# Optimization experiments

Hardware: AMD Instinct MI355X
Metric: run time of the kernel (lower is better)

## Reference

```python
import jax, jax.numpy as jnp
import numpy as np

NUM_HEADS = 8
MASK_RATE = 0.5


def setup_inputs() -> dict:
    key = jax.random.key(0)
    ks = jax.random.split(key, 6)
    B, N, C = 8, 1024, 256
    TABLE = 10
    att_embedding = jax.random.normal(ks[0], (B, N, C), dtype=jnp.float32)
    relation_position = jax.random.randint(ks[1], (B, N, N), 0, TABLE, dtype=jnp.int32)
    rel_len = jax.random.randint(ks[2], (B,), 0, 20, dtype=jnp.int32)
    W_qkv = jax.random.normal(ks[3], (C, 3 * C), dtype=jnp.float32) * (1.0 / np.sqrt(C))
    W_proj = jax.random.normal(ks[4], (C, C), dtype=jnp.float32) * (1.0 / np.sqrt(C))
    b_proj = jnp.zeros((C,), dtype=jnp.float32)
    bias_table = jax.random.normal(ks[5], (TABLE, NUM_HEADS), dtype=jnp.float32) * 0.02
    return {
        "att_embedding": att_embedding,
        "relation_position": relation_position,
        "rel_len": rel_len,
        "W_qkv": W_qkv,
        "W_proj": W_proj,
        "b_proj": b_proj,
        "bias_table": bias_table,
    }


def reference(att_embedding, relation_position, rel_len, W_qkv, W_proj, b_proj, bias_table):
    B, N, C = att_embedding.shape
    H = NUM_HEADS
    hd = C // H
    scale = hd ** -0.5

    # QKV projection (no bias): [B,N,3C] -> q,k,v each [B,H,N,hd]
    qkv = (att_embedding @ W_qkv).reshape(B, N, 3, H, hd)
    qkv = jnp.transpose(qkv, (2, 0, 3, 1, 4))
    q, k, v = qkv[0], qkv[1], qkv[2]

    # Attention scores [B,H,N,N]
    attn = jnp.einsum("bhnd,bhmd->bhnm", q, k) * scale

    # Relative position bias: gather [B,N,N,H] -> [B,H,N,N]
    pos_bias = jnp.transpose(bias_table[relation_position], (0, 3, 1, 2))

    # Mask bias: table row t gets -100 iff t > mask_len (mask_len+1 .. TABLE-1);
    # identical across heads -> compute as [B,1,N,N] instead of materializing [B,H,N,N].
    mask_len = (rel_len.astype(jnp.float32) * MASK_RATE).astype(jnp.int32)
    mask_bias = jnp.where(relation_position > mask_len[:, None, None], -100.0, 0.0)[:, None]

    attn = jax.nn.softmax(attn + pos_bias + mask_bias, axis=-1)

    # Weighted values -> [B,N,C] -> output projection
    x = jnp.einsum("bhnm,bhmd->bnhd", attn, v).reshape(B, N, C)
    x = x @ W_proj + b_proj
    return x
```

## Files before the change

kernel.cpp:

```cpp
#include <hip/hip_runtime.h>
#include <hip/hip_bf16.h>

typedef __bf16 bf16;
typedef __bf16 bf16x2 __attribute__((ext_vector_type(2)));
typedef __bf16 bf16x8 __attribute__((ext_vector_type(8)));
typedef float f32x4 __attribute__((ext_vector_type(4)));
typedef int i32x4 __attribute__((ext_vector_type(4)));

#define B_ 8
#define N_ 1024
#define C_ 256
#define H_ 8
#define C3_ 768
#define SCALE 0.17677669529663689f
#define FMAX 16.0f


__global__ __launch_bounds__(256) void prep(
    const float* __restrict__ Wqkv, const float* __restrict__ Wproj,
    bf16* __restrict__ Wq_tiled, bf16* __restrict__ Wp_tiled)
{
  int bb = blockIdx.x;
  int o = bb * 256 + threadIdx.x;
  if (bb < 768) {
    int kk = o & 31;
    int idx = o >> 5;
    int nr = idx & 63;
    int qq = idx >> 6;
    int nt = qq % 12, kt = qq / 12;
    int n = nt * 64 + nr, k = kt * 32 + kk;
    Wq_tiled[o] = (bf16)Wqkv[k * C3_ + n];
  } else {
    int p = o - 768 * 256;
    int kk = p & 31;
    int n = (p >> 5) & 255;
    int kt = p >> 13;
    int k = kt * 32 + kk;
    Wp_tiled[p] = (bf16)Wproj[k * C_ + n];
  }
}

__global__ __launch_bounds__(256) void gemm_qkv(
    const float* __restrict__ A, const bf16* __restrict__ Wq_tiled,
    bf16* __restrict__ q, bf16* __restrict__ kT, bf16* __restrict__ vT)
{
  __shared__ bf16 As[64][40];
  __shared__ bf16 Bts[64][40];
  __shared__ bf16 Vls[64][72];

  int tid = threadIdx.x;
  int wave = tid >> 6, lane = tid & 63, quad = lane >> 4, l16 = lane & 15;
  int m0 = blockIdx.x * 64, n0 = blockIdx.y * 64;
  int msub = (wave & 1) * 32, nsub = (wave >> 1) * 32;

  f32x4 acc[2][2] = {};

  int arow = tid >> 2, akc = (tid & 3) * 8;
  const float* aptr = A + (long)(m0 + arow) * C_ + akc;
  const bf16* bptr = Wq_tiled + ((long)(blockIdx.y * 64 + (tid >> 2)) * 32 + (tid & 3) * 8);

  float4 a0 = *reinterpret_cast<const float4*>(aptr);
  float4 a1 = *reinterpret_cast<const float4*>(aptr + 4);
  i32x4 bv = *reinterpret_cast<const i32x4*>(bptr);

  for (int k0 = 0; k0 < C_; k0 += 32) {
    __syncthreads();
    bf16 at[8] = {(bf16)a0.x, (bf16)a0.y, (bf16)a0.z, (bf16)a0.w,
                  (bf16)a1.x, (bf16)a1.y, (bf16)a1.z, (bf16)a1.w};
    *reinterpret_cast<bf16x8*>(&As[arow][akc]) = *reinterpret_cast<bf16x8*>(at);
    *reinterpret_cast<i32x4*>(&Bts[tid >> 2][(tid & 3) * 8]) = bv;
    __syncthreads();

    int kn = k0 + 32;
    if (kn < C_) {
      a0 = *reinterpret_cast<const float4*>(aptr + kn);
      a1 = *reinterpret_cast<const float4*>(aptr + kn + 4);
      bv = *reinterpret_cast<const i32x4*>(bptr + (long)(kn >> 5) * (12 * 64 * 32));
    }

    bf16x8 af0 = *reinterpret_cast<const bf16x8*>(&As[msub + l16][quad * 8]);
    bf16x8 af1 = *reinterpret_cast<const bf16x8*>(&As[msub + 16 + l16][quad * 8]);
    bf16x8 bfr0 = *reinterpret_cast<const bf16x8*>(&Bts[nsub + l16][quad * 8]);
    bf16x8 bfr1 = *reinterpret_cast<const bf16x8*>(&Bts[nsub + 16 + l16][quad * 8]);
    acc[0][0] = __builtin_amdgcn_mfma_f32_16x16x32_bf16(af0, bfr0, acc[0][0], 0, 0, 0);
    acc[0][1] = __builtin_amdgcn_mfma_f32_16x16x32_bf16(af0, bfr1, acc[0][1], 0, 0, 0);
    acc[1][0] = __builtin_amdgcn_mfma_f32_16x16x32_bf16(af1, bfr0, acc[1][0], 0, 0, 0);
    acc[1][1] = __builtin_amdgcn_mfma_f32_16x16x32_bf16(af1, bfr1, acc[1][1], 0, 0, 0);
  }

  if (n0 < 512) {
#pragma unroll
    for (int mi = 0; mi < 2; ++mi)
#pragma unroll
      for (int ni = 0; ni < 2; ++ni)
#pragma unroll
        for (int r = 0; r < 4; ++r) {
          int row = m0 + msub + mi * 16 + quad * 4 + r;
          int col = n0 + nsub + ni * 16 + l16;
          float v = acc[mi][ni][r];
          if (col < 256) {
            q[(long)row * 256 + col] = (bf16)v;
          } else {
            int b = row >> 10, n = row & 1023;
            int c = col - 256, h = c >> 5, d = c & 31;
            kT[(((long)(b * H_ + h)) * N_ + n) * 32 + d] = (bf16)v;
          }
        }
  } else {
    __syncthreads();
#pragma unroll
    for (int mi = 0; mi < 2; ++mi)
#pragma unroll
      for (int ni = 0; ni < 2; ++ni)
#pragma unroll
        for (int r = 0; r < 4; ++r) {
          int cc = nsub + ni * 16 + l16;
          int nn = msub + mi * 16 + quad * 4 + r;
          int np = (nn & 32) | (2 * (nn & 15)) | ((nn >> 4) & 1);
          Vls[cc][np] = (bf16)acc[mi][ni][r];
        }
    __syncthreads();
    int cc = tid >> 2, nn8 = (tid & 3) * 16;
    int b = m0 >> 10;
    long base = ((long)(b * C_ + (n0 - 512) + cc)) * N_ + (m0 & 1023) + nn8;
    *reinterpret_cast<i32x4*>(vT + base) =
        *reinterpret_cast<const i32x4*>(&Vls[cc][nn8]);
    *reinterpret_cast<i32x4*>(vT + base + 8) =
        *reinterpret_cast<const i32x4*>(&Vls[cc][nn8 + 8]);
  }
}

__global__ __launch_bounds__(512) void flash_attn(
    const bf16* __restrict__ q, const bf16* __restrict__ kT,
    const bf16* __restrict__ vT, const int* __restrict__ rel,
    const int* __restrict__ rel_len, const float* __restrict__ btab,
    float* __restrict__ att)
{
  __shared__ bf16 Vs[256][40];
  __shared__ unsigned RelsP[4][33];
  __shared__ bf16 Pls[H_][16 * 40];
  __shared__ float btl[H_][16];

  int tid = threadIdx.x;
  int h = tid >> 6, lane = tid & 63, quad = lane >> 4, l16 = lane & 15;
  int b = blockIdx.y, i0 = blockIdx.x * 16;
  long bN = (long)b * N_;

  int mask_len = (int)((float)rel_len[b] * 0.5f);
  if (tid < 80) {
    int t = tid >> 3, hh = tid & 7;
    btl[hh][t] = btab[t * H_ + hh] + (t > mask_len ? -100.f : 0.f);
  }

  bf16x8 qf = *reinterpret_cast<const bf16x8*>(
      q + (bN + i0 + l16) * 256 + h * 32 + quad * 8);

  const bf16* kbase = kT + ((long)(b * H_ + h)) * N_ * 32 + quad * 8;
  int vrow = tid >> 1, voff = (tid & 1) * 16;
  const bf16* vgp = vT + ((long)b * C_ + vrow) * N_ + voff;
  int rg = tid >> 5, rcol = tid & 31;
  const int* rgp = rel + (bN + i0 + rg * 4) * N_ + rcol;

  bf16x8 kf0 = *reinterpret_cast<const bf16x8*>(kbase + (long)l16 * 32);
  bf16x8 kf1 = *reinterpret_cast<const bf16x8*>(kbase + (long)(16 + l16) * 32);
  bf16x8 vr0 = *reinterpret_cast<const bf16x8*>(vgp);
  bf16x8 vr1 = *reinterpret_cast<const bf16x8*>(vgp + 8);
  int rr0 = 0, rr1 = 0, rr2 = 0, rr3 = 0;
  if (tid < 128) {
    rr0 = rgp[0]; rr1 = rgp[N_]; rr2 = rgp[2 * N_]; rr3 = rgp[3 * N_];
  }

  f32x4 oacc[2] = {};
  float l_part[4] = {0.f, 0.f, 0.f, 0.f};

  for (int j0 = 0; j0 < N_; j0 += 32) {
    __syncthreads();
    *reinterpret_cast<bf16x8*>(&Vs[vrow][voff]) = vr0;
    *reinterpret_cast<bf16x8*>(&Vs[vrow][voff + 8]) = vr1;
    if (tid < 128)
      RelsP[rg][rcol] = (unsigned)rr0 | ((unsigned)rr1 << 8) |
                        ((unsigned)rr2 << 16) | ((unsigned)rr3 << 24);
    __syncthreads();

    int jn = j0 + 32; jn = (jn < N_) ? jn : 0;
    bf16x8 kn0 = *reinterpret_cast<const bf16x8*>(kbase + (long)(jn + l16) * 32);
    bf16x8 kn1 = *reinterpret_cast<const bf16x8*>(kbase + (long)(jn + 16 + l16) * 32);
    vr0 = *reinterpret_cast<const bf16x8*>(vgp + jn);
    vr1 = *reinterpret_cast<const bf16x8*>(vgp + jn + 8);
    if (tid < 128) {
      rr0 = rgp[jn]; rr1 = rgp[N_ + jn]; rr2 = rgp[2 * N_ + jn]; rr3 = rgp[3 * N_ + jn];
    }

    f32x4 z = {};
    f32x4 s0 = __builtin_amdgcn_mfma_f32_16x16x32_bf16(qf, kf0, z, 0, 0, 0);
    f32x4 s1 = __builtin_amdgcn_mfma_f32_16x16x32_bf16(qf, kf1, z, 0, 0, 0);
    kf0 = kn0; kf1 = kn1;

    unsigned w0 = RelsP[quad][l16];
    unsigned w1 = RelsP[quad][16 + l16];
#pragma unroll
    for (int r = 0; r < 4; ++r) {
      int il = quad * 4 + r;
      int rv0 = (w0 >> (8 * r)) & 255;
      int rv1 = (w1 >> (8 * r)) & 255;
      float p0 = __expf(s0[r] * SCALE + btl[h][rv0] - FMAX);
      float p1 = __expf(s1[r] * SCALE + btl[h][rv1] - FMAX);
      l_part[r] += p0 + p1;
      bf16x2 pp = {(bf16)p0, (bf16)p1};
      *reinterpret_cast<bf16x2*>(&Pls[h][il * 40 + l16 * 2]) = pp;
    }
    asm volatile("s_waitcnt lgkmcnt(0)" ::: "memory");
    bf16x8 pf = *reinterpret_cast<const bf16x8*>(&Pls[h][l16 * 40 + quad * 8]);
    bf16x8 vf0 = *reinterpret_cast<const bf16x8*>(&Vs[h * 32 + l16][quad * 8]);
    bf16x8 vf1 = *reinterpret_cast<const bf16x8*>(&Vs[h * 32 + 16 + l16][quad * 8]);
    oacc[0] = __builtin_amdgcn_mfma_f32_16x16x32_bf16(pf, vf0, oacc[0], 0, 0, 0);
    oacc[1] = __builtin_amdgcn_mfma_f32_16x16x32_bf16(pf, vf1, oacc[1], 0, 0, 0);
  }

#pragma unroll
  for (int r = 0; r < 4; ++r) {
    float l = l_part[r];
#pragma unroll
    for (int m = 1; m < 16; m <<= 1) l += __shfl_xor(l, m);
    float inv = 1.f / l;
    long rowoff = (bN + i0 + quad * 4 + r) * C_ + h * 32;
    att[rowoff + l16] = oacc[0][r] * inv;
    att[rowoff + 16 + l16] = oacc[1][r] * inv;
  }
}

__global__ __launch_bounds__(256) void gemm_proj(
    const float* __restrict__ A, const bf16* __restrict__ Wp_tiled,
    const float* __restrict__ bias, float* __restrict__ Cm)
{
  __shared__ bf16 As[16][264];
  __shared__ bf16 Bts[256][40];

  int tid = threadIdx.x;
  int wave = tid >> 6, lane = tid & 63, quad = lane >> 4, l16 = lane & 15;
  int m0 = blockIdx.x * 16;

  {
    int row = tid >> 4, c0 = (tid & 15) * 16;
#pragma unroll
    for (int j8 = 0; j8 < 2; ++j8) {
      float4 v0 = *reinterpret_cast<const float4*>(A + (long)(m0 + row) * C_ + c0 + j8 * 8);
      float4 v1 = *reinterpret_cast<const float4*>(A + (long)(m0 + row) * C_ + c0 + j8 * 8 + 4);
      bf16 at[8] = {(bf16)v0.x, (bf16)v0.y, (bf16)v0.z, (bf16)v0.w,
                    (bf16)v1.x, (bf16)v1.y, (bf16)v1.z, (bf16)v1.w};
      *reinterpret_cast<bf16x8*>(&As[row][c0 + j8 * 8]) = *reinterpret_cast<bf16x8*>(at);
    }
  }

  f32x4 acc[4] = {};
  const bf16* wp = Wp_tiled + (long)tid * 32;

  i32x4 bv0 = *reinterpret_cast<const i32x4*>(wp);
  i32x4 bv1 = *reinterpret_cast<const i32x4*>(wp + 8);
  i32x4 bv2 = *reinterpret_cast<const i32x4*>(wp + 16);
  i32x4 bv3 = *reinterpret_cast<const i32x4*>(wp + 24);

  for (int k0 = 0; k0 < C_; k0 += 32) {
    __syncthreads();
    *reinterpret_cast<i32x4*>(&Bts[tid][0]) = bv0;
    *reinterpret_cast<i32x4*>(&Bts[tid][8]) = bv1;
    *reinterpret_cast<i32x4*>(&Bts[tid][16]) = bv2;
    *reinterpret_cast<i32x4*>(&Bts[tid][24]) = bv3;
    __syncthreads();

    int kn = k0 + 32;
    if (kn < C_) {
      long off = (long)(kn >> 5) * 8192;
      bv0 = *reinterpret_cast<const i32x4*>(wp + off);
      bv1 = *reinterpret_cast<const i32x4*>(wp + off + 8);
      bv2 = *reinterpret_cast<const i32x4*>(wp + off + 16);
      bv3 = *reinterpret_cast<const i32x4*>(wp + off + 24);
    }

    bf16x8 af = *reinterpret_cast<const bf16x8*>(&As[l16][k0 + quad * 8]);
#pragma unroll
    for (int ni = 0; ni < 4; ++ni) {
      bf16x8 bfr = *reinterpret_cast<const bf16x8*>(
          &Bts[wave * 64 + ni * 16 + l16][quad * 8]);
      acc[ni] = __builtin_amdgcn_mfma_f32_16x16x32_bf16(af, bfr, acc[ni], 0, 0, 0);
    }
  }

#pragma unroll
  for (int ni = 0; ni < 4; ++ni)
#pragma unroll
    for (int r = 0; r < 4; ++r) {
      int row = m0 + quad * 4 + r;
      int col = wave * 64 + ni * 16 + l16;
      Cm[(long)row * C_ + col] = acc[ni][r] + bias[col];
    }
}

extern "C" void kernel_launch(void* const* d_in, const int* in_sizes, int n_in,
                              void* d_out, int out_size, void* d_ws, size_t ws_size,
                              hipStream_t stream) {
  const float* X     = (const float*)d_in[0];
  const int*   rel   = (const int*)d_in[1];
  const int*   rlen  = (const int*)d_in[2];
  const float* Wqkv  = (const float*)d_in[3];
  const float* Wproj = (const float*)d_in[4];
  const float* bproj = (const float*)d_in[5];
  const float* btab  = (const float*)d_in[6];
  float* out = (float*)d_out;

  char* ws = (char*)d_ws;
  bf16* Wq_tiled = (bf16*)ws;
  bf16* Wp_tiled = (bf16*)(ws + 393216);
  bf16* q  = (bf16*)(ws + 524288);
  bf16* kT = (bf16*)(ws + 524288 + 4194304);
  bf16* vT = (bf16*)(ws + 524288 + 2 * 4194304);

  prep<<<dim3(1024), 256, 0, stream>>>(Wqkv, Wproj, Wq_tiled, Wp_tiled);
  gemm_qkv<<<dim3(8192 / 64, C3_ / 64), 256, 0, stream>>>(X, Wq_tiled, q, kT, vT);
  flash_attn<<<dim3(N_ / 16, B_), 512, 0, stream>>>(q, kT, vT, rel, rlen, btab, out);
  gemm_proj<<<dim3(8192 / 16), 256, 0, stream>>>(out, Wp_tiled, bproj, out);
}
```

Before: 143.1 us.

## Split attention blocks by head group and double-buffer V/rel tiles in LDS

The attention kernel now launches two 256-thread blocks per query tile, each covering four heads, instead of one 512-thread block covering all eight. V and packed relation-index tiles are double-buffered in shared memory, so each loop iteration needs one barrier instead of two. The next tile is written to the alternate buffer after the current tile's MFMAs. This adds parallelism and cuts sync overhead, but each head-group block reloads the full relation-position tile, doubling that global read traffic.

```diff
diff --git a/kernel.cpp b/kernel.cpp
--- a/kernel.cpp
+++ b/kernel.cpp
@@ -130,20 +130,21 @@
   }
 }
 
-__global__ __launch_bounds__(512) void flash_attn(
+__global__ __launch_bounds__(256) void flash_attn(
     const bf16* __restrict__ q, const bf16* __restrict__ kT,
     const bf16* __restrict__ vT, const int* __restrict__ rel,
     const int* __restrict__ rel_len, const float* __restrict__ btab,
     float* __restrict__ att)
 {
-  __shared__ bf16 Vs[256][40];
-  __shared__ unsigned RelsP[4][33];
-  __shared__ bf16 Pls[H_][16 * 40];
+  __shared__ bf16 Vs[2][128][40];
+  __shared__ unsigned RelsP[2][4][33];
+  __shared__ bf16 Pls[4][16 * 40];
   __shared__ float btl[H_][16];
 
   int tid = threadIdx.x;
-  int h = tid >> 6, lane = tid & 63, quad = lane >> 4, l16 = lane & 15;
-  int b = blockIdx.y, i0 = blockIdx.x * 16;
+  int wv = tid >> 6, lane = tid & 63, quad = lane >> 4, l16 = lane & 15;
+  int b = blockIdx.y, i0 = blockIdx.x * 16, hg = blockIdx.z;
+  int h = hg * 4 + wv;
   long bN = (long)b * N_;
 
   int mask_len = (int)((float)rel_len[b] * 0.5f);
@@ -157,47 +158,49 @@
 
   const bf16* kbase = kT + ((long)(b * H_ + h)) * N_ * 32 + quad * 8;
   int vrow = tid >> 1, voff = (tid & 1) * 16;
-  const bf16* vgp = vT + ((long)b * C_ + vrow) * N_ + voff;
-  int rg = tid >> 5, rcol = tid & 31;
+  const bf16* vgp = vT + ((long)b * C_ + hg * 128 + vrow) * N_ + voff;
+  int rg = (tid >> 5) & 3, rcol = tid & 31;
   const int* rgp = rel + (bN + i0 + rg * 4) * N_ + rcol;
 
   bf16x8 kf0 = *reinterpret_cast<const bf16x8*>(kbase + (long)l16 * 32);
   bf16x8 kf1 = *reinterpret_cast<const bf16x8*>(kbase + (long)(16 + l16) * 32);
-  bf16x8 vr0 = *reinterpret_cast<const bf16x8*>(vgp);
-  bf16x8 vr1 = *reinterpret_cast<const bf16x8*>(vgp + 8);
-  int rr0 = 0, rr1 = 0, rr2 = 0, rr3 = 0;
-  if (tid < 128) {
-    rr0 = rgp[0]; rr1 = rgp[N_]; rr2 = rgp[2 * N_]; rr3 = rgp[3 * N_];
-  }
+  {
+    bf16x8 v0 = *reinterpret_cast<const bf16x8*>(vgp);
+    bf16x8 v1 = *reinterpret_cast<const bf16x8*>(vgp + 8);
+    *reinterpret_cast<bf16x8*>(&Vs[0][vrow][voff]) = v0;
+    *reinterpret_cast<bf16x8*>(&Vs[0][vrow][voff + 8]) = v1;
+    if (tid < 128) {
+      unsigned p = (unsigned)rgp[0] | ((unsigned)rgp[N_] << 8) |
+                   ((unsigned)rgp[2 * N_] << 16) | ((unsigned)rgp[3 * N_] << 24);
+      RelsP[0][rg][rcol] = p;
+    }
+  }
+  __syncthreads();
 
   f32x4 oacc[2] = {};
   float l_part[4] = {0.f, 0.f, 0.f, 0.f};
 
-  for (int j0 = 0; j0 < N_; j0 += 32) {
-    __syncthreads();
-    *reinterpret_cast<bf16x8*>(&Vs[vrow][voff]) = vr0;
-    *reinterpret_cast<bf16x8*>(&Vs[vrow][voff + 8]) = vr1;
-    if (tid < 128)
-      RelsP[rg][rcol] = (unsigned)rr0 | ((unsigned)rr1 << 8) |
-                        ((unsigned)rr2 << 16) | ((unsigned)rr3 << 24);
-    __syncthreads();
+  for (int it = 0; it < 32; ++it) {
+    int j0 = it * 32;
+    int cb = it & 1, nb = cb ^ 1;
 
     int jn = j0 + 32; jn = (jn < N_) ? jn : 0;
     bf16x8 kn0 = *reinterpret_cast<const bf16x8*>(kbase + (long)(jn + l16) * 32);
     bf16x8 kn1 = *reinterpret_cast<const bf16x8*>(kbase + (long)(jn + 16 + l16) * 32);
-    vr0 = *reinterpret_cast<const bf16x8*>(vgp + jn);
-    vr1 = *reinterpret_cast<const bf16x8*>(vgp + jn + 8);
+    bf16x8 vn0 = *reinterpret_cast<const bf16x8*>(vgp + jn);
+    bf16x8 vn1 = *reinterpret_cast<const bf16x8*>(vgp + jn + 8);
+    int rr0 = 0, rr1 = 0, rr2 = 0, rr3 = 0;
     if (tid < 128) {
-      rr0 = rgp[jn]; rr1 = rgp[N_ + jn]; rr2 = rgp[2 * N_ + jn]; rr3 = rgp[3 * N_ + jn];
+      rr0 = rgp[jn]; rr1 = rgp[N_ + jn];
+      rr2 = rgp[2 * N_ + jn]; rr3 = rgp[3 * N_ + jn];
     }
 
     f32x4 z = {};
     f32x4 s0 = __builtin_amdgcn_mfma_f32_16x16x32_bf16(qf, kf0, z, 0, 0, 0);
     f32x4 s1 = __builtin_amdgcn_mfma_f32_16x16x32_bf16(qf, kf1, z, 0, 0, 0);
-    kf0 = kn0; kf1 = kn1;
-
-    unsigned w0 = RelsP[quad][l16];
-    unsigned w1 = RelsP[quad][16 + l16];
+
+    unsigned w0 = RelsP[cb][quad][l16];
+    unsigned w1 = RelsP[cb][quad][16 + l16];
 #pragma unroll
     for (int r = 0; r < 4; ++r) {
       int il = quad * 4 + r;
@@ -207,14 +210,23 @@
       float p1 = __expf(s1[r] * SCALE + btl[h][rv1] - FMAX);
       l_part[r] += p0 + p1;
       bf16x2 pp = {(bf16)p0, (bf16)p1};
-      *reinterpret_cast<bf16x2*>(&Pls[h][il * 40 + l16 * 2]) = pp;
+      *reinterpret_cast<bf16x2*>(&Pls[wv][il * 40 + l16 * 2]) = pp;
     }
     asm volatile("s_waitcnt lgkmcnt(0)" ::: "memory");
-    bf16x8 pf = *reinterpret_cast<const bf16x8*>(&Pls[h][l16 * 40 + quad * 8]);
-    bf16x8 vf0 = *reinterpret_cast<const bf16x8*>(&Vs[h * 32 + l16][quad * 8]);
-    bf16x8 vf1 = *reinterpret_cast<const bf16x8*>(&Vs[h * 32 + 16 + l16][quad * 8]);
+    bf16x8 pf = *reinterpret_cast<const bf16x8*>(&Pls[wv][l16 * 40 + quad * 8]);
+    bf16x8 vf0 = *reinterpret_cast<const bf16x8*>(&Vs[cb][wv * 32 + l16][quad * 8]);
+    bf16x8 vf1 = *reinterpret_cast<const bf16x8*>(&Vs[cb][wv * 32 + 16 + l16][quad * 8]);
     oacc[0] = __builtin_amdgcn_mfma_f32_16x16x32_bf16(pf, vf0, oacc[0], 0, 0, 0);
     oacc[1] = __builtin_amdgcn_mfma_f32_16x16x32_bf16(pf, vf1, oacc[1], 0, 0, 0);
+
+    *reinterpret_cast<bf16x8*>(&Vs[nb][vrow][voff]) = vn0;
+    *reinterpret_cast<bf16x8*>(&Vs[nb][vrow][voff + 8]) = vn1;
+    if (tid < 128)
+      RelsP[nb][rg][rcol] = (unsigned)rr0 | ((unsigned)rr1 << 8) |
+                            ((unsigned)rr2 << 16) | ((unsigned)rr3 << 24);
+    kf0 = kn0; kf1 = kn1;
+
+    __syncthreads();
   }
 
 #pragma unroll
@@ -317,6 +329,6 @@
 
   prep<<<dim3(1024), 256, 0, stream>>>(Wqkv, Wproj, Wq_tiled, Wp_tiled);
   gemm_qkv<<<dim3(8192 / 64, C3_ / 64), 256, 0, stream>>>(X, Wq_tiled, q, kT, vT);
-  flash_attn<<<dim3(N_ / 16, B_), 512, 0, stream>>>(q, kT, vT, rel, rlen, btab, out);
+  flash_attn<<<dim3(N_ / 16, B_, 2), 256, 0, stream>>>(q, kT, vT, rel, rlen, btab, out);
   gemm_proj<<<dim3(8192 / 16), 256, 0, stream>>>(out, Wp_tiled, bproj, out);
 }
```

New measurement: 148.5 us. 3.8% more time.
